# Optimization experiments

Hardware: AMD Instinct MI355X
Metric: run time of the kernel (lower is better)

The kernel has to match this reference:

```python
import jax, jax.numpy as jnp
import numpy as np

N_QUBITS = 8
N_LAYERS = 2
FILTERS = 2
K = 2  # kernelsize


def _rx(theta):
    # RX(theta) = [[cos(t/2), -i sin(t/2)], [-i sin(t/2), cos(t/2)]]
    c = jnp.cos(theta / 2)
    s = jnp.sin(theta / 2)
    row0 = jnp.stack([c + 0j, -1j * s])
    row1 = jnp.stack([-1j * s, c + 0j])
    return jnp.stack([row0, row1]).astype(jnp.complex64)


def _apply_1q(state, U, q):
    # state: (2,)*n complex
    state = jnp.moveaxis(state, q, 0)
    state = jnp.tensordot(U, state, axes=[[1], [0]])
    return jnp.moveaxis(state, 0, q)


_CNOT = jnp.array([[1, 0, 0, 0],
                   [0, 1, 0, 0],
                   [0, 0, 0, 1],
                   [0, 0, 1, 0]], dtype=jnp.complex64)


def _apply_cnot(state, c, t):
    n = state.ndim
    state = jnp.moveaxis(state, (c, t), (0, 1))
    shp = state.shape
    state = state.reshape(4, -1)
    state = _CNOT @ state
    state = state.reshape(shp)
    return jnp.moveaxis(state, (0, 1), (c, t))


def _circuit(feat, weights):
    # feat: (K*K,) patch values; weights: (N_LAYERS, N_QUBITS)
    n = N_QUBITS
    state = jnp.zeros((2,) * n, dtype=jnp.complex64).at[(0,) * n].set(1.0)
    # AngleEmbedding (RX) on first K*K wires
    for i in range(K * K):
        state = _apply_1q(state, _rx(feat[i]), i)
    # BasicEntanglerLayers: RX on every wire, then ring of CNOTs
    for l in range(N_LAYERS):
        for q in range(n):
            state = _apply_1q(state, _rx(weights[l, q]), q)
        for q in range(n):
            state = _apply_cnot(state, q, (q + 1) % n)
    probs = jnp.abs(state) ** 2  # (2,)*n real
    z = []
    for q in range(n):
        pq = jnp.moveaxis(probs, q, 0)
        z.append(pq[0].sum() - pq[1].sum())  # expval PauliZ_q
    return jnp.stack(z)  # (n,)


def setup_inputs() -> dict:
    key = jax.random.key(0)
    k1, k2 = jax.random.split(key)
    x = jax.random.normal(k1, (8, 3, 40, 40), dtype=jnp.float32)
    weights = jax.random.normal(k2, (N_LAYERS, N_QUBITS), dtype=jnp.float32)
    return {"x": x, "weights": weights}


def reference(x, weights):
    bs, ch, h, w = x.shape
    h_out = (h - K) // 1 + 1
    w_out = (w - K) // 1 + 1
    # sliding-window patches: (bs, ch, h_out, w_out, K*K)
    patches = jnp.stack(
        [x[:, :, dj:dj + h_out, dk:dk + w_out] for dj in range(K) for dk in range(K)],
        axis=-1,
    )
    feats = patches.reshape(-1, K * K)  # (N, K*K)
    q = jax.vmap(_circuit, in_axes=(0, None))(feats, weights)  # (N, N_QUBITS)
    out = q[:, :FILTERS].reshape(bs, ch, h_out, w_out, FILTERS)
    out = out.mean(axis=1)  # channel-sum then /ch
    out = jnp.moveaxis(out, -1, 1)  # (bs, FILTERS, h_out, w_out)
    return out.astype(jnp.float32)
```

## Files before the change

### kernel.cpp

```cpp
#include <hip/hip_runtime.h>


namespace {

template<int M>
__device__ __forceinline__ void rx_local(float (&sr)[16], float (&si)[16], float c, float s) {
#pragma unroll
    for (int r = 0; r < 16; ++r) {
        if (r & M) continue;
        const int a = r, b = r | M;
        float nra = c*sr[a] + s*si[b], nia = c*si[a] - s*sr[b];
        float nrb = c*sr[b] + s*si[a], nib = c*si[b] - s*sr[a];
        sr[a]=nra; si[a]=nia; sr[b]=nrb; si[b]=nib;
    }
}

__device__ __forceinline__ void rx_lane16(float (&sr)[16], float (&si)[16], float c, float s, int mask) {
#pragma unroll
    for (int r = 0; r < 16; ++r) {
        float orr = __shfl_xor(sr[r], mask, 64);
        float oii = __shfl_xor(si[r], mask, 64);
        sr[r] = c*sr[r] + s*oii;
        si[r] = c*si[r] - s*orr;
    }
}

template<int C, int T>
__device__ __forceinline__ void cnot_ll(float (&sr)[16], float (&si)[16]) {
#pragma unroll
    for (int r = 0; r < 16; ++r) {
        if (!(r & C) || (r & T)) continue;
        const int a = r, b = r ^ T;
        float tr=sr[a], ti=si[a];
        sr[a]=sr[b]; si[a]=si[b];
        sr[b]=tr;    si[b]=ti;
    }
}

__device__ __forceinline__ void entangler(float (&sr)[16], float (&si)[16],
                                          const float* __restrict__ w, int lane) {
    float c, s;
#pragma unroll
    for (int l = 0; l < 2; ++l) {
        __sincosf(0.5f*w[l*8+0], &s, &c); rx_local<1>(sr, si, c, s);
        __sincosf(0.5f*w[l*8+1], &s, &c); rx_local<2>(sr, si, c, s);
        __sincosf(0.5f*w[l*8+2], &s, &c); rx_local<4>(sr, si, c, s);
        __sincosf(0.5f*w[l*8+3], &s, &c); rx_local<8>(sr, si, c, s);
        __sincosf(0.5f*w[l*8+4], &s, &c); rx_lane16(sr, si, c, s, 1);
        __sincosf(0.5f*w[l*8+5], &s, &c); rx_lane16(sr, si, c, s, 2);
        __sincosf(0.5f*w[l*8+6], &s, &c); rx_lane16(sr, si, c, s, 4);
        __sincosf(0.5f*w[l*8+7], &s, &c); rx_lane16(sr, si, c, s, 8);

        cnot_ll<1,2>(sr, si);
        cnot_ll<2,4>(sr, si);
        cnot_ll<4,8>(sr, si);
#pragma unroll
        for (int r = 8; r < 16; ++r) {
            sr[r] = __shfl_xor(sr[r], 1, 64);
            si[r] = __shfl_xor(si[r], 1, 64);
        }
#pragma unroll
        for (int qq = 0; qq < 3; ++qq) {
            const int mt = 2 << qq;
            const bool ctrl = (lane >> qq) & 1;
#pragma unroll
            for (int r = 0; r < 16; ++r) {
                float orr = __shfl_xor(sr[r], mt, 64);
                float oii = __shfl_xor(si[r], mt, 64);
                sr[r] = ctrl ? orr : sr[r];
                si[r] = ctrl ? oii : si[r];
            }
        }
        {
            const bool c7 = (lane >> 3) & 1;
#pragma unroll
            for (int r = 0; r < 16; r += 2) {
                float ar = c7 ? sr[r+1] : sr[r];
                float ai = c7 ? si[r+1] : si[r];
                float br = c7 ? sr[r]   : sr[r+1];
                float bi = c7 ? si[r]   : si[r+1];
                sr[r]=ar; si[r]=ai; sr[r+1]=br; si[r+1]=bi;
            }
        }
    }
}

__device__ __forceinline__ int uidx(int n, int g) { return n*16 + g + (n>>4); }

__device__ __forceinline__ void tri_decode(int t, int& rr, int& rp) {
    int r = 0, rem = t;
    while (rem >= 16 - r) { rem -= 16 - r; ++r; }
    rr = r; rp = r + rem;
}

__device__ __forceinline__ int ilv(int bra, int ket) {
    int idx = 0;
#pragma unroll
    for (int k = 0; k < 4; ++k)
        idx |= (((bra>>k)&1) << (2*k+1)) | (((ket>>k)&1) << (2*k));
    return idx;
}

}

#define NPIX (8*39*39)
#define BLK  1024
#define PPB  512
#define NBLK ((NPIX + PPB - 1) / PPB)

__global__ __launch_bounds__(1024) void quanv_fused(
    const float* __restrict__ x,
    const float* __restrict__ w,
    float* __restrict__ out)
{
    __shared__ float2 U[16*256 + 16];
    __shared__ float2 XA[2][256];
    __shared__ float2 XB[2][256];
    __shared__ float2 PB[4][2][136];
    __shared__ __align__(16) float Tp[216];

    const int tid  = (int)threadIdx.x;
    const int lane = tid & 63;

    const int half = tid >> 9;
    const int gpix = (int)blockIdx.x * PPB + (tid & 511);
    const int pid  = (gpix < NPIX) ? gpix : (NPIX - 1);
    const int j  = pid % 39;
    const int t2 = pid / 39;
    const int i  = t2 % 39;
    const int b  = t2 / 39;

    float f[12];
#pragma unroll
    for (int c = 0; c < 3; ++c) {
        const float* xp = x + (((b*3 + c)*40) + i)*40 + j;
        f[c*4+0] = xp[0];  f[c*4+1] = xp[1];
        f[c*4+2] = xp[40]; f[c*4+3] = xp[41];
    }

    if (tid < 256) {
        const int g = (tid >> 6) * 4 + (lane >> 4);
        float sr[16], si[16];
#pragma unroll
        for (int r = 0; r < 16; ++r) {
            sr[r] = (((lane & 15) == 0) && (r == g)) ? 1.f : 0.f;
            si[r] = 0.f;
        }
        entangler(sr, si, w, lane);
#pragma unroll
        for (int r = 0; r < 16; ++r) {
            const int n = ((lane & 15) << 4) | r;
            U[uidx(n, g)] = make_float2(sr[r], si[r]);
        }
    }
    __syncthreads();

    if (tid < 544) {
        const int t = tid >> 2, quarter = tid & 3;
        int rr, rp; tri_decode(t, rr, rp);
        float2 a0={0,0}, a1={0,0}, a2={0,0}, a3={0,0};
        const int n0 = quarter * 64;
        for (int n = n0; n < n0 + 64; n += 4) {
#pragma unroll
            for (int cls = 0; cls < 4; ++cls) {
                const float2 ur = U[uidx(n+cls, rr)];
                const float2 up = U[uidx(n+cls, rp)];
                const float cre = ur.x*up.x + ur.y*up.y;
                const float cim = ur.x*up.y - ur.y*up.x;
                if      (cls==0) { a0.x += cre; a0.y += cim; }
                else if (cls==1) { a1.x += cre; a1.y += cim; }
                else if (cls==2) { a2.x += cre; a2.y += cim; }
                else             { a3.x += cre; a3.y += cim; }
            }
        }
        PB[quarter][0][t] = make_float2((a0.x - a1.x) + (a2.x - a3.x),
                                        (a0.y - a1.y) + (a2.y - a3.y));
        PB[quarter][1][t] = make_float2((a0.x + a1.x) - (a2.x + a3.x),
                                        (a0.y + a1.y) - (a2.y + a3.y));
    }
    __syncthreads();

    if (tid < 136) {
        int rr, rp; tri_decode(tid, rr, rp);
        const int idx  = ilv(rr, rp);
        const int idxT = ilv(rp, rr);
#pragma unroll
        for (int q = 0; q < 2; ++q) {
            float2 m = PB[0][q][tid];
            m.x += PB[1][q][tid].x + PB[2][q][tid].x + PB[3][q][tid].x;
            m.y += PB[1][q][tid].y + PB[2][q][tid].y + PB[3][q][tid].y;
            XA[q][idxT] = make_float2(m.x, -m.y);
            XA[q][idx]  = m;
        }
    }
    __syncthreads();

    float2 (*A)[256] = XA;
    float2 (*B)[256] = XB;
    for (int k = 0; k < 4; ++k) {
        if (tid < 128) {
            const int q = tid >> 6, quad = tid & 63;
            const int st = 1 << (2*k);
            const int ml = st - 1;
            const int base = (quad & ml) | ((quad & ~ml) << 2);
            const float2 i00 = A[q][base],      i01 = A[q][base+st];
            const float2 i10 = A[q][base+2*st], i11 = A[q][base+3*st];
            B[q][base]      = make_float2(0.5f*(i00.x+i11.x), 0.5f*(i00.y+i11.y));
            B[q][base+st]   = make_float2(0.5f*(i01.x+i10.x), 0.5f*(i01.y+i10.y));
            B[q][base+2*st] = make_float2(-0.5f*(i01.y-i10.y), 0.5f*(i01.x-i10.x));
            B[q][base+3*st] = make_float2(0.5f*(i00.x-i11.x), 0.5f*(i00.y-i11.y));
        }
        __syncthreads();
        float2 (*t)[256] = A; A = B; B = t;
    }

    if (tid < 162) {
        const int q = tid / 81, u = tid % 81;
        const int i0 = u % 3, i1 = (u/3) % 3, i2 = (u/9) % 3, i3 = u / 27;
        const int p0 = (i0==0)?0:(i0+1);
        const int p1 = (i1==0)?0:(i1+1);
        const int p2 = (i2==0)?0:(i2+1);
        const int p3 = (i3==0)?0:(i3+1);
        const int idx = p0 | (p1<<2) | (p2<<4) | (p3<<6);
        Tp[q*108 + (u/3)*4 + i0] = A[q][idx].x * (1.f/3.f);
    }
    __syncthreads();

    if (gpix < NPIX) {
        float vy[3][4], vz[3][4];
#pragma unroll
        for (int c = 0; c < 3; ++c) {
#pragma unroll
            for (int k = 0; k < 4; ++k) {
                float s, co;
                __sincosf(f[c*4+k], &s, &co);
                vy[c][k] = -s; vz[c][k] = co;
            }
        }

        float a3[3] = {0.f, 0.f, 0.f};
#pragma unroll
        for (int i3 = 0; i3 < 3; ++i3) {
            float a2[3] = {0.f, 0.f, 0.f};
#pragma unroll
            for (int i2 = 0; i2 < 3; ++i2) {
                float a1[3] = {0.f, 0.f, 0.f};
#pragma unroll
                for (int i1 = 0; i1 < 3; ++i1) {
                    const float4 tv = *reinterpret_cast<const float4*>(
                        &Tp[half*108 + ((i3*3 + i2)*3 + i1)*4]);
#pragma unroll
                    for (int c = 0; c < 3; ++c) {
                        const float s = fmaf(tv.z, vz[c][0], fmaf(tv.y, vy[c][0], tv.x));
                        if      (i1 == 0) a1[c] += s;
                        else if (i1 == 1) a1[c] = fmaf(s, vy[c][1], a1[c]);
                        else              a1[c] = fmaf(s, vz[c][1], a1[c]);
                    }
                }
#pragma unroll
                for (int c = 0; c < 3; ++c) {
                    if      (i2 == 0) a2[c] += a1[c];
                    else if (i2 == 1) a2[c] = fmaf(a1[c], vy[c][2], a2[c]);
                    else              a2[c] = fmaf(a1[c], vz[c][2], a2[c]);
                }
            }
#pragma unroll
            for (int c = 0; c < 3; ++c) {
                if      (i3 == 0) a3[c] += a2[c];
                else if (i3 == 1) a3[c] = fmaf(a2[c], vy[c][3], a3[c]);
                else              a3[c] = fmaf(a2[c], vz[c][3], a3[c]);
            }
        }

        out[((b*2 + half)*39 + i)*39 + j] = a3[0] + a3[1] + a3[2];
    }
}

extern "C" void kernel_launch(void* const* d_in, const int* in_sizes, int n_in,
                              void* d_out, int out_size, void* d_ws, size_t ws_size,
                              hipStream_t stream) {
    const float* x = (const float*)d_in[0];
    const float* w = (const float*)d_in[1];
    float* out = (float*)d_out;

    quanv_fused<<<NBLK, BLK, 0, stream>>>(x, w, out);
}
```

Measured before the change: 20.84 us.

## Spread entangler unitary simulation across all 16 waves with 4 amplitudes per lane

The per-block simulation of the 16 entangler columns moves from 4 waves holding 16 amplitudes per lane to all 16 waves, each simulating one basis column with 4 amplitudes per lane across 64 lanes. Most qubit gates and CNOTs therefore become cross-lane shuffles on fewer registers, which shortens the serial critical path before the first barrier. The sincos of the pixel features is also moved ahead of the unitary build so it overlaps with it. The cost is more shuffle traffic in total and higher register pressure from holding vy/vz across the prologue.

```diff
diff --git a/kernel.cpp b/kernel.cpp
--- a/kernel.cpp
+++ b/kernel.cpp
@@ -3,21 +3,28 @@
 
 namespace {
 
-template<int M>
-__device__ __forceinline__ void rx_local(float (&sr)[16], float (&si)[16], float c, float s) {
-#pragma unroll
-    for (int r = 0; r < 16; ++r) {
-        if (r & M) continue;
-        const int a = r, b = r | M;
-        float nra = c*sr[a] + s*si[b], nia = c*si[a] - s*sr[b];
-        float nrb = c*sr[b] + s*si[a], nib = c*si[b] - s*sr[a];
-        sr[a]=nra; si[a]=nia; sr[b]=nrb; si[b]=nib;
-    }
-}
-
-__device__ __forceinline__ void rx_lane16(float (&sr)[16], float (&si)[16], float c, float s, int mask) {
-#pragma unroll
-    for (int r = 0; r < 16; ++r) {
+
+__device__ __forceinline__ void rx_l0(float (&sr)[4], float (&si)[4], float c, float s) {
+    float nr0 = c*sr[0] + s*si[1], ni0 = c*si[0] - s*sr[1];
+    float nr1 = c*sr[1] + s*si[0], ni1 = c*si[1] - s*sr[0];
+    float nr2 = c*sr[2] + s*si[3], ni2 = c*si[2] - s*sr[3];
+    float nr3 = c*sr[3] + s*si[2], ni3 = c*si[3] - s*sr[2];
+    sr[0]=nr0; si[0]=ni0; sr[1]=nr1; si[1]=ni1;
+    sr[2]=nr2; si[2]=ni2; sr[3]=nr3; si[3]=ni3;
+}
+
+__device__ __forceinline__ void rx_l1(float (&sr)[4], float (&si)[4], float c, float s) {
+    float nr0 = c*sr[0] + s*si[2], ni0 = c*si[0] - s*sr[2];
+    float nr2 = c*sr[2] + s*si[0], ni2 = c*si[2] - s*sr[0];
+    float nr1 = c*sr[1] + s*si[3], ni1 = c*si[1] - s*sr[3];
+    float nr3 = c*sr[3] + s*si[1], ni3 = c*si[3] - s*sr[1];
+    sr[0]=nr0; si[0]=ni0; sr[1]=nr1; si[1]=ni1;
+    sr[2]=nr2; si[2]=ni2; sr[3]=nr3; si[3]=ni3;
+}
+
+__device__ __forceinline__ void rx_lane4(float (&sr)[4], float (&si)[4], float c, float s, int mask) {
+#pragma unroll
+    for (int r = 0; r < 4; ++r) {
         float orr = __shfl_xor(sr[r], mask, 64);
         float oii = __shfl_xor(si[r], mask, 64);
         sr[r] = c*sr[r] + s*oii;
@@ -25,62 +32,45 @@
     }
 }
 
-template<int C, int T>
-__device__ __forceinline__ void cnot_ll(float (&sr)[16], float (&si)[16]) {
-#pragma unroll
-    for (int r = 0; r < 16; ++r) {
-        if (!(r & C) || (r & T)) continue;
-        const int a = r, b = r ^ T;
-        float tr=sr[a], ti=si[a];
-        sr[a]=sr[b]; si[a]=si[b];
-        sr[b]=tr;    si[b]=ti;
-    }
-}
-
-__device__ __forceinline__ void entangler(float (&sr)[16], float (&si)[16],
-                                          const float* __restrict__ w, int lane) {
+__device__ __forceinline__ void entangler64(float (&sr)[4], float (&si)[4],
+                                            const float* __restrict__ w, int lane) {
     float c, s;
 #pragma unroll
     for (int l = 0; l < 2; ++l) {
-        __sincosf(0.5f*w[l*8+0], &s, &c); rx_local<1>(sr, si, c, s);
-        __sincosf(0.5f*w[l*8+1], &s, &c); rx_local<2>(sr, si, c, s);
-        __sincosf(0.5f*w[l*8+2], &s, &c); rx_local<4>(sr, si, c, s);
-        __sincosf(0.5f*w[l*8+3], &s, &c); rx_local<8>(sr, si, c, s);
-        __sincosf(0.5f*w[l*8+4], &s, &c); rx_lane16(sr, si, c, s, 1);
-        __sincosf(0.5f*w[l*8+5], &s, &c); rx_lane16(sr, si, c, s, 2);
-        __sincosf(0.5f*w[l*8+6], &s, &c); rx_lane16(sr, si, c, s, 4);
-        __sincosf(0.5f*w[l*8+7], &s, &c); rx_lane16(sr, si, c, s, 8);
-
-        cnot_ll<1,2>(sr, si);
-        cnot_ll<2,4>(sr, si);
-        cnot_ll<4,8>(sr, si);
-#pragma unroll
-        for (int r = 8; r < 16; ++r) {
-            sr[r] = __shfl_xor(sr[r], 1, 64);
-            si[r] = __shfl_xor(si[r], 1, 64);
-        }
-#pragma unroll
-        for (int qq = 0; qq < 3; ++qq) {
-            const int mt = 2 << qq;
-            const bool ctrl = (lane >> qq) & 1;
-#pragma unroll
-            for (int r = 0; r < 16; ++r) {
+        __sincosf(0.5f*w[l*8+0], &s, &c); rx_l0(sr, si, c, s);
+        __sincosf(0.5f*w[l*8+1], &s, &c); rx_l1(sr, si, c, s);
+#pragma unroll
+        for (int q = 2; q < 8; ++q) {
+            __sincosf(0.5f*w[l*8+q], &s, &c);
+            rx_lane4(sr, si, c, s, 1 << (q-2));
+        }
+
+        { float tr=sr[1], ti=si[1]; sr[1]=sr[3]; si[1]=si[3]; sr[3]=tr; si[3]=ti; }
+
+        sr[2] = __shfl_xor(sr[2], 1, 64); si[2] = __shfl_xor(si[2], 1, 64);
+        sr[3] = __shfl_xor(sr[3], 1, 64); si[3] = __shfl_xor(si[3], 1, 64);
+
+#pragma unroll
+        for (int q = 2; q <= 6; ++q) {
+            const int mt = 1 << (q-1);
+            const bool ctrl = (lane >> (q-2)) & 1;
+#pragma unroll
+            for (int r = 0; r < 4; ++r) {
                 float orr = __shfl_xor(sr[r], mt, 64);
                 float oii = __shfl_xor(si[r], mt, 64);
                 sr[r] = ctrl ? orr : sr[r];
                 si[r] = ctrl ? oii : si[r];
             }
         }
+
         {
-            const bool c7 = (lane >> 3) & 1;
-#pragma unroll
-            for (int r = 0; r < 16; r += 2) {
-                float ar = c7 ? sr[r+1] : sr[r];
-                float ai = c7 ? si[r+1] : si[r];
-                float br = c7 ? sr[r]   : sr[r+1];
-                float bi = c7 ? si[r]   : si[r+1];
-                sr[r]=ar; si[r]=ai; sr[r+1]=br; si[r+1]=bi;
-            }
+            const bool ctrl = (lane >> 5) & 1;
+            float a0 = ctrl ? sr[1] : sr[0], b0 = ctrl ? si[1] : si[0];
+            float a1 = ctrl ? sr[0] : sr[1], b1 = ctrl ? si[0] : si[1];
+            float a2 = ctrl ? sr[3] : sr[2], b2 = ctrl ? si[3] : si[2];
+            float a3 = ctrl ? sr[2] : sr[3], b3 = ctrl ? si[2] : si[3];
+            sr[0]=a0; si[0]=b0; sr[1]=a1; si[1]=b1;
+            sr[2]=a2; si[2]=b2; sr[3]=a3; si[3]=b3;
         }
     }
 }
@@ -121,6 +111,7 @@
 
     const int tid  = (int)threadIdx.x;
     const int lane = tid & 63;
+    const int wv   = tid >> 6;
 
     const int half = tid >> 9;
     const int gpix = (int)blockIdx.x * PPB + (tid & 511);
@@ -130,27 +121,32 @@
     const int i  = t2 % 39;
     const int b  = t2 / 39;
 
-    float f[12];
+    float vy[3][4], vz[3][4];
 #pragma unroll
     for (int c = 0; c < 3; ++c) {
         const float* xp = x + (((b*3 + c)*40) + i)*40 + j;
-        f[c*4+0] = xp[0];  f[c*4+1] = xp[1];
-        f[c*4+2] = xp[40]; f[c*4+3] = xp[41];
-    }
-
-    if (tid < 256) {
-        const int g = (tid >> 6) * 4 + (lane >> 4);
-        float sr[16], si[16];
-#pragma unroll
-        for (int r = 0; r < 16; ++r) {
-            sr[r] = (((lane & 15) == 0) && (r == g)) ? 1.f : 0.f;
+        const float f0 = xp[0], f1 = xp[1], f2 = xp[40], f3 = xp[41];
+        float s, co;
+        __sincosf(f0, &s, &co); vy[c][0] = -s; vz[c][0] = co;
+        __sincosf(f1, &s, &co); vy[c][1] = -s; vz[c][1] = co;
+        __sincosf(f2, &s, &co); vy[c][2] = -s; vz[c][2] = co;
+        __sincosf(f3, &s, &co); vy[c][3] = -s; vz[c][3] = co;
+    }
+
+    {
+        float sr[4], si[4];
+        const int lane0 = (wv >> 2) & 3;
+        const int r0    = wv & 3;
+#pragma unroll
+        for (int r = 0; r < 4; ++r) {
+            sr[r] = (lane == lane0 && r == r0) ? 1.f : 0.f;
             si[r] = 0.f;
         }
-        entangler(sr, si, w, lane);
-#pragma unroll
-        for (int r = 0; r < 16; ++r) {
-            const int n = ((lane & 15) << 4) | r;
-            U[uidx(n, g)] = make_float2(sr[r], si[r]);
+        entangler64(sr, si, w, lane);
+#pragma unroll
+        for (int r = 0; r < 4; ++r) {
+            const int n = (lane << 2) | r;
+            U[uidx(n, wv)] = make_float2(sr[r], si[r]);
         }
     }
     __syncthreads();
@@ -227,17 +223,6 @@
     __syncthreads();
 
     if (gpix < NPIX) {
-        float vy[3][4], vz[3][4];
-#pragma unroll
-        for (int c = 0; c < 3; ++c) {
-#pragma unroll
-            for (int k = 0; k < 4; ++k) {
-                float s, co;
-                __sincosf(f[c*4+k], &s, &co);
-                vy[c][k] = -s; vz[c][k] = co;
-            }
-        }
-
         float a3[3] = {0.f, 0.f, 0.f};
 #pragma unroll
         for (int i3 = 0; i3 < 3; ++i3) {
```

Measured after the change: 26.94 us. 1.29x slower.
